# Performance work log

Hardware: AMD Instinct MI355X
Metric: run time of the kernel (lower is better)

The kernel has to match this reference:

```python
import jax, jax.numpy as jnp
import numpy as np

DIM = 512; LAYERS = 6; K = 15; VOCAB = 32000; B = 2; L = 1024
HID = 1024  # SwiGLU hidden: int(512*2) rounded up to multiple of 64
RANK = 64; BLOCK = 2048; MIX_W = 0.1
UP_DIL = [1, 2, 4, 8, 16, 32]
DN_DIL = UP_DIL[::-1]


def rmsnorm(x, w, eps=1e-6):
    return x * jax.lax.rsqrt(jnp.mean(x * x, axis=-1, keepdims=True) + eps) * w


def dconv(x, w, b, dil):
    # x: [B,D,T]; w: [D,1,K] depthwise; left (causal) padding of (K-1)*dil
    pad = (w.shape[-1] - 1) * dil
    y = jax.lax.conv_general_dilated(
        x, w, window_strides=(1,), padding=[(pad, 0)], rhs_dilation=(dil,),
        dimension_numbers=('NCH', 'OIH', 'NCH'), feature_group_count=x.shape[1])
    return y + b[None, :, None]


def conv_block(x, nw, cw, cb, w1, w2, w3, dil):
    # CausalDilatedConv: RMSNorm -> depthwise causal dilated conv -> silu -> SwiGLU -> +residual
    h = rmsnorm(x, nw)
    h = jax.nn.silu(dconv(jnp.transpose(h, (0, 2, 1)), cw, cb, dil))
    h = jnp.transpose(h, (0, 2, 1))
    h = jnp.einsum('bth,dh->btd',
                   jax.nn.silu(jnp.einsum('btd,hd->bth', h, w1)) * jnp.einsum('btd,hd->bth', h, w3),
                   w2)
    return h + x


def run_stack(x, dils, nw, cw, cb, w1, w2, w3, kp, ki, kd, gnorm):
    integral = x; previous = x; current = x
    for i, d in enumerate(dils):
        if i > 0:
            # PIDGate: step == i >= 1 so max(step,1) == i
            pid = kp[i-1] * current + ki[i-1] * (integral / i) + kd[i-1] * (current - previous)
            cur_in = rmsnorm(jax.nn.silu(pid), gnorm[i-1])
        else:
            cur_in = current
        current = conv_block(cur_in, nw[i], cw[i], cb[i], w1[i], w2[i], w3[i], d)
        previous = current
        integral = integral + current
    return current


def mix(x):
    # CausalMeanPool: x + 0.1 * causal running mean
    counts = jnp.arange(1, x.shape[1] + 1, dtype=x.dtype)[None, :, None]
    return x + MIX_W * jnp.cumsum(x, axis=1) / counts


def sgate(new, old, nw, dw, db, uw, ub):
    h = jax.nn.silu(rmsnorm(new, nw) @ dw.T + db)
    g = jax.nn.sigmoid(h @ uw.T + ub)
    return g * new + (1.0 - g) * old


def setup_inputs() -> dict:
    key = jax.random.key(0)
    ks = iter(jax.random.split(key, 64))
    def nrm(shape, s=0.02):
        return jax.random.normal(next(ks), shape, jnp.float32) * s
    def stack_params(p):
        return {
            p + '_norm_w': jnp.ones((LAYERS, DIM), jnp.float32),
            p + '_conv_w': nrm((LAYERS, DIM, 1, K), 0.1),
            p + '_conv_b': jnp.zeros((LAYERS, DIM), jnp.float32),
            p + '_w1': nrm((LAYERS, HID, DIM)),
            p + '_w2': nrm((LAYERS, DIM, HID)),
            p + '_w3': nrm((LAYERS, HID, DIM)),
            p + '_kp': jnp.full((LAYERS - 1, DIM), 0.5, jnp.float32),
            p + '_ki': jnp.full((LAYERS - 1, DIM), 0.3, jnp.float32),
            p + '_kd': jnp.full((LAYERS - 1, DIM), 0.2, jnp.float32),
            p + '_gnorm': jnp.ones((LAYERS - 1, DIM), jnp.float32),
        }
    inp = {
        'idx': jax.random.randint(next(ks), (B, L), 0, VOCAB),
        'emb': nrm((VOCAB, DIM)),
        'pos': nrm((1, BLOCK, DIM)),
        'emb_norm_w': jnp.ones((DIM,), jnp.float32),
        'token_shift': jnp.full((DIM,), 0.5, jnp.float32),
        'mem_gate_w': jnp.zeros((DIM, DIM), jnp.float32),  # nn.init.zeros_
        'mem_gate_b': nrm((DIM,)),
        'memory_p': jnp.zeros((B, DIM), jnp.float32),  # buffer, zero after reset()
        'sg_norm': jnp.ones((3, DIM), jnp.float32),
        'sg_down_w': nrm((3, RANK, DIM)),
        'sg_down_b': jnp.zeros((3, RANK), jnp.float32),
        'sg_up_w': nrm((3, DIM, RANK)),
        'sg_up_b': jnp.zeros((3, DIM), jnp.float32),
        'final_norm_w': jnp.ones((DIM,), jnp.float32),
    }
    inp.update(stack_params('up'))
    inp.update(stack_params('dn'))
    return inp


def _forward(idx, emb, pos, emb_norm_w, token_shift, mem_gate_w, mem_gate_b, memory_p,
             up_norm_w, up_conv_w, up_conv_b, up_w1, up_w2, up_w3, up_kp, up_ki, up_kd, up_gnorm,
             dn_norm_w, dn_conv_w, dn_conv_b, dn_w1, dn_w2, dn_w3, dn_kp, dn_ki, dn_kd, dn_gnorm,
             sg_norm, sg_down_w, sg_down_b, sg_up_w, sg_up_b, final_norm_w):
    T = idx.shape[1]
    x = emb[idx] + pos[:, :T]
    x = rmsnorm(x, emb_norm_w)
    # dropout is identity at eval time
    # memory injection: token-shift mix + sigmoid-gated persistent P-memory
    shifted = jnp.concatenate(
        [x[:, :1], token_shift * x[:, :-1] + (1.0 - token_shift) * x[:, 1:]], axis=1)
    mem = jax.nn.sigmoid(memory_p @ mem_gate_w.T + mem_gate_b)
    x = shifted + mem[:, None, :]
    initial = x
    up_p = (up_norm_w, up_conv_w, up_conv_b, up_w1, up_w2, up_w3, up_kp, up_ki, up_kd, up_gnorm)
    dn_p = (dn_norm_w, dn_conv_w, dn_conv_b, dn_w1, dn_w2, dn_w3, dn_kp, dn_ki, dn_kd, dn_gnorm)
    up1 = mix(run_stack(x, UP_DIL, *up_p))
    gated1 = sgate(up1, initial, sg_norm[0], sg_down_w[0], sg_down_b[0], sg_up_w[0], sg_up_b[0])
    down = mix(run_stack(gated1, DN_DIL, *dn_p))
    gated2 = sgate(down, initial, sg_norm[1], sg_down_w[1], sg_down_b[1], sg_up_w[1], sg_up_b[1])
    up2 = mix(run_stack(gated2, UP_DIL, *up_p))  # up_stack weights are shared/reused
    output = sgate(up2, gated2, sg_norm[2], sg_down_w[2], sg_down_b[2], sg_up_w[2], sg_up_b[2])
    output = rmsnorm(output, final_norm_w)
    return output @ emb.T  # tied head


def reference(idx, emb, pos, emb_norm_w, token_shift, mem_gate_w, mem_gate_b, memory_p,
              up_norm_w, up_conv_w, up_conv_b, up_w1, up_w2, up_w3, up_kp, up_ki, up_kd, up_gnorm,
              dn_norm_w, dn_conv_w, dn_conv_b, dn_w1, dn_w2, dn_w3, dn_kp, dn_ki, dn_kd, dn_gnorm,
              sg_norm, sg_down_w, sg_down_b, sg_up_w, sg_up_b, final_norm_w):
    return _forward(idx, emb, pos, emb_norm_w, token_shift, mem_gate_w, mem_gate_b, memory_p,
                    up_norm_w, up_conv_w, up_conv_b, up_w1, up_w2, up_w3, up_kp, up_ki, up_kd, up_gnorm,
                    dn_norm_w, dn_conv_w, dn_conv_b, dn_w1, dn_w2, dn_w3, dn_kp, dn_ki, dn_kd, dn_gnorm,
                    sg_norm, sg_down_w, sg_down_b, sg_up_w, sg_up_b, final_norm_w)
```

## Files before the change

### kernel.cpp

```cpp
#include <hip/hip_runtime.h>
#include <math.h>

#define DIM 512
#define NLAYERS 6
#define KSZ 15
#define VOCAB 32000
#define BATCH 2
#define SEQ 1024
#define HIDN 1024
#define RANK 64
#define NTOK (BATCH*SEQ)
#define MIXW 0.1f

typedef unsigned short u16;
typedef _Float16 f16;
typedef _Float16 f16x8 __attribute__((ext_vector_type(8)));
typedef _Float16 f16x4 __attribute__((ext_vector_type(4)));
typedef float  f32x4  __attribute__((ext_vector_type(4)));

__device__ __forceinline__ float sigm(float x){ return 1.f/(1.f+__expf(-x)); }

__device__ __forceinline__ float wred(float v){
  #pragma unroll
  for (int o=32;o>0;o>>=1) v += __shfl_xor(v, o, 64);
  return v;
}

#define MFMA16(a,b,c) __builtin_amdgcn_mfma_f32_16x16x32_f16(a,b,c,0,0,0)

__device__ __forceinline__ void gld16(const f16* g, f16* l){
  __builtin_amdgcn_global_load_lds(
      (const __attribute__((address_space(1))) void*)g,
      (__attribute__((address_space(3))) void*)l, 16, 0, 0);
}

__global__ __launch_bounds__(256) void k_cvt(const float* __restrict__ s,
    f16* __restrict__ d, long n4){
  long i = (long)blockIdx.x*256 + threadIdx.x;
  if (i >= n4) return;
  float4 v = reinterpret_cast<const float4*>(s)[i];
  f16x4 o; o.x=(f16)v.x; o.y=(f16)v.y; o.z=(f16)v.z; o.w=(f16)v.w;
  reinterpret_cast<f16x4*>(d)[i] = o;
}

__global__ __launch_bounds__(256) void k_cvtconv(const float* __restrict__ cw,
    float* __restrict__ cwT, int n){
  int i = blockIdx.x*256 + threadIdx.x;
  if (i >= n) return;
  int d = i & (DIM-1); int m = (i >> 9) % KSZ; int l = i / (KSZ*DIM);
  cwT[i] = cw[((size_t)l*DIM + d)*KSZ + (KSZ-1-m)];
}

__global__ __launch_bounds__(64) void k_embnorm(const int* __restrict__ idx,
    const float* __restrict__ emb, const float* __restrict__ pos,
    const float* __restrict__ w, float* __restrict__ out){
  int row = blockIdx.x;
  int t = row & (SEQ-1);
  int lane = threadIdx.x;
  long ebase = (long)idx[row]*DIM;
  long pbase = (long)t*DIM;
  float v[8]; float ss = 0.f;
  #pragma unroll
  for (int c=0;c<2;c++){
    int d = c*256 + lane*4;
    float4 e = *reinterpret_cast<const float4*>(emb + ebase + d);
    float4 p = *reinterpret_cast<const float4*>(pos + pbase + d);
    float x0 = e.x+p.x, x1 = e.y+p.y, x2 = e.z+p.z, x3 = e.w+p.w;
    v[c*4+0]=x0; v[c*4+1]=x1; v[c*4+2]=x2; v[c*4+3]=x3;
    ss += x0*x0 + x1*x1 + x2*x2 + x3*x3;
  }
  ss = wred(ss);
  float rs = rsqrtf(ss*(1.f/DIM) + 1e-6f);
  long ob = (long)row*DIM;
  #pragma unroll
  for (int c=0;c<2;c++){
    int d = c*256 + lane*4;
    float4 wv = *reinterpret_cast<const float4*>(w + d);
    float4 o;
    o.x = v[c*4+0]*rs*wv.x; o.y = v[c*4+1]*rs*wv.y;
    o.z = v[c*4+2]*rs*wv.z; o.w = v[c*4+3]*rs*wv.w;
    *reinterpret_cast<float4*>(out + ob + d) = o;
  }
}

__global__ void k_mem(const float* __restrict__ p, const float* __restrict__ gw,
                      const float* __restrict__ gb, float* __restrict__ mem){
  int i = blockIdx.x*blockDim.x + threadIdx.x;
  if (i >= BATCH*DIM) return;
  int b = i >> 9, d = i & (DIM-1);
  float acc = gb[d];
  const float* wr = gw + (long)d*DIM;
  const float* pr = p + b*DIM;
  for (int k=0;k<DIM;k+=4){
    float4 wv = *reinterpret_cast<const float4*>(wr+k);
    float4 pv = *reinterpret_cast<const float4*>(pr+k);
    acc += wv.x*pv.x + wv.y*pv.y + wv.z*pv.z + wv.w*pv.w;
  }
  mem[i] = sigm(acc);
}

__global__ void k_shift(const float* __restrict__ xn, const float* __restrict__ mem,
    const float* __restrict__ ts, float* __restrict__ out){
  int i = blockIdx.x*256 + threadIdx.x;
  int d = i & (DIM-1); int row = i >> 9; int t = row & (SEQ-1); int b = row >> 10;
  float cur = xn[i];
  float v;
  if (t == 0) v = cur;
  else { float f = ts[d]; v = f*xn[i-DIM] + (1.f-f)*cur; }
  out[i] = v + mem[b*DIM + d];
}

__global__ __launch_bounds__(64) void k_rms(const float* __restrict__ x,
    const float* __restrict__ w, f16* __restrict__ oh){
  int row = blockIdx.x; int lane = threadIdx.x;
  const float* xr = x + (long)row*DIM;
  float v[8]; float ss = 0.f;
  #pragma unroll
  for (int c=0;c<2;c++){
    int d = c*256 + lane*4;
    float4 f = *reinterpret_cast<const float4*>(xr + d);
    v[c*4+0]=f.x; v[c*4+1]=f.y; v[c*4+2]=f.z; v[c*4+3]=f.w;
    ss += f.x*f.x + f.y*f.y + f.z*f.z + f.w*f.w;
  }
  ss = wred(ss);
  float rs = rsqrtf(ss*(1.f/DIM) + 1e-6f);
  long ob = (long)row*DIM;
  #pragma unroll
  for (int c=0;c<2;c++){
    int d = c*256 + lane*4;
    float4 wv = *reinterpret_cast<const float4*>(w + d);
    f16x4 o;
    o.x = (f16)(v[c*4+0]*rs*wv.x); o.y = (f16)(v[c*4+1]*rs*wv.y);
    o.z = (f16)(v[c*4+2]*rs*wv.z); o.w = (f16)(v[c*4+3]*rs*wv.w);
    *reinterpret_cast<f16x4*>(oh + ob + d) = o;
  }
}

__global__ __launch_bounds__(64) void k_pid(const float* __restrict__ C,
    const float* __restrict__ I, float inv_i,
    const float* __restrict__ kp, const float* __restrict__ ki,
    const float* __restrict__ gn, const float* __restrict__ nw,
    float* __restrict__ xin, f16* __restrict__ oh){
  int row = blockIdx.x; int lane = threadIdx.x;
  long base = (long)row*DIM;
  float u[8]; float ss = 0.f;
  #pragma unroll
  for (int c=0;c<2;c++){
    int d = c*256 + lane*4;
    float4 cv = *reinterpret_cast<const float4*>(C + base + d);
    float4 iv = *reinterpret_cast<const float4*>(I + base + d);
    float4 kpv = *reinterpret_cast<const float4*>(kp + d);
    float4 kiv = *reinterpret_cast<const float4*>(ki + d);
    float p0 = kpv.x*cv.x + kiv.x*(iv.x*inv_i);
    float p1 = kpv.y*cv.y + kiv.y*(iv.y*inv_i);
    float p2 = kpv.z*cv.z + kiv.z*(iv.z*inv_i);
    float p3 = kpv.w*cv.w + kiv.w*(iv.w*inv_i);
    float s0 = p0*sigm(p0), s1 = p1*sigm(p1), s2 = p2*sigm(p2), s3 = p3*sigm(p3);
    u[c*4+0]=s0; u[c*4+1]=s1; u[c*4+2]=s2; u[c*4+3]=s3;
    ss += s0*s0 + s1*s1 + s2*s2 + s3*s3;
  }
  ss = wred(ss);
  float rs1 = rsqrtf(ss*(1.f/DIM) + 1e-6f);
  float x2[8]; float ss2 = 0.f;
  #pragma unroll
  for (int c=0;c<2;c++){
    int d = c*256 + lane*4;
    float4 gv = *reinterpret_cast<const float4*>(gn + d);
    float y0 = u[c*4+0]*rs1*gv.x, y1 = u[c*4+1]*rs1*gv.y;
    float y2 = u[c*4+2]*rs1*gv.z, y3 = u[c*4+3]*rs1*gv.w;
    x2[c*4+0]=y0; x2[c*4+1]=y1; x2[c*4+2]=y2; x2[c*4+3]=y3;
    ss2 += y0*y0 + y1*y1 + y2*y2 + y3*y3;
    float4 o; o.x=y0; o.y=y1; o.z=y2; o.w=y3;
    *reinterpret_cast<float4*>(xin + base + d) = o;
  }
  ss2 = wred(ss2);
  float rs2 = rsqrtf(ss2*(1.f/DIM) + 1e-6f);
  #pragma unroll
  for (int c=0;c<2;c++){
    int d = c*256 + lane*4;
    float4 nv = *reinterpret_cast<const float4*>(nw + d);
    f16x4 o;
    o.x = (f16)(x2[c*4+0]*rs2*nv.x); o.y = (f16)(x2[c*4+1]*rs2*nv.y);
    o.z = (f16)(x2[c*4+2]*rs2*nv.z); o.w = (f16)(x2[c*4+3]*rs2*nv.w);
    *reinterpret_cast<f16x4*>(oh + base + d) = o;
  }
}

__global__ void k_conv(const f16* __restrict__ h1,
    const float* __restrict__ cwT, const float* __restrict__ cb,
    f16* __restrict__ hc, int dil){
  int i = blockIdx.x*256 + threadIdx.x;
  int d = i & (DIM-1); int row = i >> 9; int t = row & (SEQ-1);
  float acc = cb[d];
  #pragma unroll
  for (int m=0;m<KSZ;m++){
    if (t - m*dil >= 0) acc += cwT[m*DIM + d] * (float)h1[i - m*dil*DIM];
  }
  float s = acc * sigm(acc);
  hc[i] = (f16)s;
}

template<int BM,int KD,int EPI>
__global__ __launch_bounds__(256) void k_mm(
    const f16* __restrict__ A, const f16* __restrict__ B0, const f16* __restrict__ B1,
    const float* __restrict__ XIN, float* __restrict__ OF, float* __restrict__ I,
    f16* __restrict__ OH){
  constexpr int WM = BM/4, MF = WM/16, NF = 4;
  constexpr int NMAT = (EPI==0) ? 2 : 1;
  constexpr int ATILE = BM*64;
  constexpr int BTILE = NMAT*64*64;
  constexpr int STRIDE = ATILE + BTILE;
  constexpr int AI = (BM/4)/8;
  constexpr int NT = KD/64;
  __shared__ f16 smem[2*STRIDE];
  int tid = threadIdx.x;
  int lane = tid & 63, wid = tid >> 6;
  int m0, n0;
  if constexpr (EPI==2){ int bid = blockIdx.x; m0 = (bid&15)*BM; n0 = (bid>>4)*64; }
  else { m0 = blockIdx.x*BM; n0 = blockIdx.y*64; }

  int lrow = lane >> 3, slot = lane & 7;

  auto stage = [&](int buf, int k0){
    f16* sA = smem + buf*STRIDE;
    f16* sB = sA + ATILE;
    #pragma unroll
    for (int j=0;j<AI;j++){
      int rowb = wid*(BM/4) + j*8;
      int row = rowb + lrow;
      gld16(A + (size_t)(m0+row)*KD + k0 + ((slot^(row&7))*8), sA + rowb*64);
    }
    #pragma unroll
    for (int j=0;j<2;j++){
      int rowb = wid*16 + j*8;
      int row = rowb + lrow;
      gld16(B0 + (size_t)(n0+row)*KD + k0 + ((slot^(row&7))*8), sB + rowb*64);
      if constexpr (EPI==0)
        gld16(B1 + (size_t)(n0+row)*KD + k0 + ((slot^(row&7))*8), sB + 4096 + rowb*64);
    }
  };

  f32x4 acc0[MF][NF] = {};
  f32x4 acc1[(EPI==0)?MF:1][(EPI==0)?NF:1] = {};

  stage(0, 0);
  __syncthreads();
  for (int t=0;t<NT;t++){
    int cur = t & 1;
    if (t+1 < NT) stage(cur^1, (t+1)*64);
    const f16* sA = smem + cur*STRIDE;
    const f16* sB = sA + ATILE;
    #pragma unroll
    for (int kk=0;kk<2;kk++){
      int kp0 = kk*4 + (lane>>4);
      f16x8 af[MF], bf[NF], bg[(EPI==0)?NF:1];
      #pragma unroll
      for (int mf=0;mf<MF;mf++){
        int row = wid*WM + mf*16 + (lane&15);
        af[mf] = *reinterpret_cast<const f16x8*>(&sA[row*64 + (kp0^(row&7))*8]);
      }
      #pragma unroll
      for (int nf=0;nf<NF;nf++){
        int row = nf*16 + (lane&15);
        bf[nf] = *reinterpret_cast<const f16x8*>(&sB[row*64 + (kp0^(row&7))*8]);
        if constexpr (EPI==0)
          bg[nf] = *reinterpret_cast<const f16x8*>(&sB[4096 + row*64 + (kp0^(row&7))*8]);
      }
      #pragma unroll
      for (int mf=0;mf<MF;mf++){
        #pragma unroll
        for (int nf=0;nf<NF;nf++){
          acc0[mf][nf] = MFMA16(af[mf], bf[nf], acc0[mf][nf]);
          if constexpr (EPI==0)
            acc1[mf][nf] = MFMA16(af[mf], bg[nf], acc1[mf][nf]);
        }
      }
    }
    __syncthreads();
  }

  float* stg = (float*)smem + wid*(16*68);
  int dr = (lane>>4)*4, dc = lane&15;
  #pragma unroll
  for (int mf=0;mf<MF;mf++){
    #pragma unroll
    for (int nf=0;nf<NF;nf++){
      #pragma unroll
      for (int q=0;q<4;q++){
        float v;
        if constexpr (EPI==0){
          float x1 = acc0[mf][nf][q];
          v = x1*sigm(x1)*acc1[mf][nf][q];
        } else v = acc0[mf][nf][q];
        stg[(dr+q)*68 + nf*16 + dc] = v;
      }
    }
    int gmb = m0 + wid*WM + mf*16;
    if constexpr (EPI==0){
      #pragma unroll
      for (int pass=0;pass<2;pass++){
        int r = pass*8 + (lane>>3);
        int c = 8*(lane&7);
        float4 lo = *reinterpret_cast<float4*>(&stg[r*68 + c]);
        float4 hi = *reinterpret_cast<float4*>(&stg[r*68 + c + 4]);
        f16x8 o;
        o[0]=(f16)lo.x; o[1]=(f16)lo.y; o[2]=(f16)lo.z; o[3]=(f16)lo.w;
        o[4]=(f16)hi.x; o[5]=(f16)hi.y; o[6]=(f16)hi.z; o[7]=(f16)hi.w;
        *reinterpret_cast<f16x8*>(&OH[(size_t)(gmb+r)*HIDN + n0 + c]) = o;
      }
    } else if constexpr (EPI==1){
      #pragma unroll
      for (int pass=0;pass<4;pass++){
        int r = pass*4 + (lane>>4);
        int c = 4*(lane&15);
        float4 v = *reinterpret_cast<float4*>(&stg[r*68 + c]);
        size_t o = (size_t)(gmb+r)*DIM + n0 + c;
        float4 x = *reinterpret_cast<const float4*>(&XIN[o]);
        v.x += x.x; v.y += x.y; v.z += x.z; v.w += x.w;
        *reinterpret_cast<float4*>(&OF[o]) = v;
        float4 iv = *reinterpret_cast<const float4*>(&I[o]);
        iv.x += v.x; iv.y += v.y; iv.z += v.z; iv.w += v.w;
        *reinterpret_cast<float4*>(&I[o]) = iv;
      }
    } else {
      #pragma unroll
      for (int pass=0;pass<4;pass++){
        int r = pass*4 + (lane>>4);
        int c = 4*(lane&15);
        float4 v = *reinterpret_cast<float4*>(&stg[r*68 + c]);
        *reinterpret_cast<float4*>(&OF[(size_t)(gmb+r)*VOCAB + n0 + c]) = v;
      }
    }
  }
}

__global__ __launch_bounds__(64) void k_mix(float* __restrict__ x){
  int col = blockIdx.x;
  int b = col >> 9, d = col & (DIM-1);
  int lane = threadIdx.x;
  long o = (long)b*SEQ*DIM + d + (long)lane*16*DIM;
  float v[16]; float s = 0.f;
  #pragma unroll
  for (int j=0;j<16;j++){ v[j] = x[o + (long)j*DIM]; s += v[j]; }
  float t = s;
  #pragma unroll
  for (int off=1; off<64; off<<=1){
    float u = __shfl_up(t, off, 64);
    if (lane >= off) t += u;
  }
  float run = t - s;
  #pragma unroll
  for (int j=0;j<16;j++){
    run += v[j];
    int tt = lane*16 + j;
    x[o + (long)j*DIM] = v[j] + MIXW*run/(float)(tt+1);
  }
}

__global__ __launch_bounds__(256) void k_sgate(const float* __restrict__ xnew,
    const float* __restrict__ xold, const float* __restrict__ nw,
    const float* __restrict__ dw, const float* __restrict__ db,
    const float* __restrict__ uw, const float* __restrict__ ub,
    float* __restrict__ out){
  __shared__ float raw[DIM];
  __shared__ float xn[DIM];
  __shared__ float part[256];
  __shared__ float hb[RANK];
  int row = blockIdx.x, tid = threadIdx.x;
  long base = (long)row*DIM;
  float ss = 0.f;
  for (int d=tid; d<DIM; d+=256){ float v = xnew[base+d]; raw[d]=v; ss += v*v; }
  ss = wred(ss);
  if ((tid&63)==0) part[tid>>6] = ss;
  __syncthreads();
  float tot = part[0]+part[1]+part[2]+part[3];
  float rs = rsqrtf(tot*(1.f/DIM)+1e-6f);
  for (int d=tid; d<DIM; d+=256) xn[d] = raw[d]*rs*nw[d];
  __syncthreads();
  int rr = tid & 63, q = tid >> 6;
  float p = 0.f;
  const float* dwr = dw + (long)rr*DIM + q*128;
  const float* xq = xn + q*128;
  #pragma unroll 8
  for (int d=0; d<128; d+=4){
    float4 wv = *reinterpret_cast<const float4*>(dwr+d);
    p += xq[d]*wv.x + xq[d+1]*wv.y + xq[d+2]*wv.z + xq[d+3]*wv.w;
  }
  part[tid] = p;
  __syncthreads();
  if (tid < RANK){
    float h = part[tid] + part[64+tid] + part[128+tid] + part[192+tid] + db[tid];
    hb[tid] = h * sigm(h);
  }
  __syncthreads();
  for (int d=tid; d<DIM; d+=256){
    float a = ub[d];
    const float* ur = uw + (long)d*RANK;
    #pragma unroll
    for (int rj=0;rj<RANK;rj+=4){
      float4 uv = *reinterpret_cast<const float4*>(ur+rj);
      a += hb[rj]*uv.x + hb[rj+1]*uv.y + hb[rj+2]*uv.z + hb[rj+3]*uv.w;
    }
    float g = sigm(a);
    out[base+d] = g*raw[d] + (1.f-g)*xold[base+d];
  }
}

extern "C" void kernel_launch(void* const* d_in, const int* in_sizes, int n_in,
                              void* d_out, int out_size, void* d_ws, size_t ws_size,
                              hipStream_t stream){
  const int*   idx           = (const int*)d_in[0];
  const float* emb           = (const float*)d_in[1];
  const float* pos           = (const float*)d_in[2];
  const float* emb_norm_w    = (const float*)d_in[3];
  const float* token_shift   = (const float*)d_in[4];
  const float* mem_gate_w    = (const float*)d_in[5];
  const float* mem_gate_b    = (const float*)d_in[6];
  const float* memory_p      = (const float*)d_in[7];
  const float* sg_norm       = (const float*)d_in[8];
  const float* sg_down_w     = (const float*)d_in[9];
  const float* sg_down_b     = (const float*)d_in[10];
  const float* sg_up_w       = (const float*)d_in[11];
  const float* sg_up_b       = (const float*)d_in[12];
  const float* final_norm_w  = (const float*)d_in[13];
  struct StackP { const float *nw, *cw, *cb, *w1, *w2, *w3, *kp, *ki, *gn; };
  StackP up { (const float*)d_in[14], (const float*)d_in[15], (const float*)d_in[16],
              (const float*)d_in[17], (const float*)d_in[18], (const float*)d_in[19],
              (const float*)d_in[20], (const float*)d_in[21], (const float*)d_in[23] };
  StackP dn { (const float*)d_in[24], (const float*)d_in[25], (const float*)d_in[26],
              (const float*)d_in[27], (const float*)d_in[28], (const float*)d_in[29],
              (const float*)d_in[30], (const float*)d_in[31], (const float*)d_in[33] };

  char* wp = (char*)d_ws;
  auto alloc = [&](size_t bytes)->void*{
    void* p = (void*)wp; wp += (bytes + 255) & ~(size_t)255; return p;
  };
  float* A0  = (float*)alloc((size_t)NTOK*DIM*4);
  float* A1  = (float*)alloc((size_t)NTOK*DIM*4);
  float* Cb  = (float*)alloc((size_t)NTOK*DIM*4);
  float* Ib  = (float*)alloc((size_t)NTOK*DIM*4);
  float* XIN = (float*)alloc((size_t)NTOK*DIM*4);
  f16*   H1  = (f16*)alloc((size_t)NTOK*DIM*2);
  f16*   HC  = (f16*)alloc((size_t)NTOK*DIM*2);
  f16*   G   = (f16*)alloc((size_t)NTOK*HIDN*2);
  const size_t WSZ = (size_t)NLAYERS*HIDN*DIM;
  f16*   UpW1 = (f16*)alloc(WSZ*2);
  f16*   UpW2 = (f16*)alloc(WSZ*2);
  f16*   UpW3 = (f16*)alloc(WSZ*2);
  f16*   DnW1 = (f16*)alloc(WSZ*2);
  f16*   DnW2 = (f16*)alloc(WSZ*2);
  f16*   DnW3 = (f16*)alloc(WSZ*2);
  f16*   Ef   = (f16*)alloc((size_t)VOCAB*DIM*2);
  float* UpCT = (float*)alloc((size_t)NLAYERS*KSZ*DIM*4);
  float* DnCT = (float*)alloc((size_t)NLAYERS*KSZ*DIM*4);
  float* MEM  = (float*)alloc((size_t)BATCH*DIM*4);

  static const int updil[NLAYERS] = {1,2,4,8,16,32};
  static const int dndil[NLAYERS] = {32,16,8,4,2,1};

  {
    long n4 = WSZ/4;
    int g = (int)((n4 + 255)/256);
    k_cvt<<<g,256,0,stream>>>(up.w1, UpW1, n4);
    k_cvt<<<g,256,0,stream>>>(up.w2, UpW2, n4);
    k_cvt<<<g,256,0,stream>>>(up.w3, UpW3, n4);
    k_cvt<<<g,256,0,stream>>>(dn.w1, DnW1, n4);
    k_cvt<<<g,256,0,stream>>>(dn.w2, DnW2, n4);
    k_cvt<<<g,256,0,stream>>>(dn.w3, DnW3, n4);
    long e4 = (long)VOCAB*DIM/4;
    k_cvt<<<(int)((e4+255)/256),256,0,stream>>>(emb, Ef, e4);
    int nc = NLAYERS*KSZ*DIM;
    k_cvtconv<<<(nc+255)/256,256,0,stream>>>(up.cw, UpCT, nc);
    k_cvtconv<<<(nc+255)/256,256,0,stream>>>(dn.cw, DnCT, nc);
  }

  k_embnorm<<<NTOK,64,0,stream>>>(idx, emb, pos, emb_norm_w, Cb);
  k_mem<<<(BATCH*DIM+255)/256,256,0,stream>>>(memory_p, mem_gate_w, mem_gate_b, MEM);
  k_shift<<<NTOK*DIM/256,256,0,stream>>>(Cb, MEM, token_shift, A0);

  auto run_stack = [&](const float* xs, const StackP& S, const float* CT,
                       const f16* W1f, const f16* W2f, const f16* W3f, const int* dil){
    hipMemcpyAsync(Ib, xs, (size_t)NTOK*DIM*4, hipMemcpyDeviceToDevice, stream);
    for (int l=0;l<NLAYERS;l++){
      const float* bin;
      if (l==0){
        bin = xs;
        k_rms<<<NTOK,64,0,stream>>>(xs, S.nw + l*DIM, H1);
      } else {
        k_pid<<<NTOK,64,0,stream>>>(Cb, Ib, 1.f/(float)l,
            S.kp+(l-1)*DIM, S.ki+(l-1)*DIM, S.gn+(l-1)*DIM, S.nw+l*DIM, XIN, H1);
        bin = XIN;
      }
      k_conv<<<NTOK*DIM/256,256,0,stream>>>(H1, CT + (size_t)l*KSZ*DIM, S.cb + l*DIM, HC, dil[l]);
      k_mm<128,512,0><<<dim3(NTOK/128, HIDN/64),256,0,stream>>>(
          HC, W1f + (size_t)l*HIDN*DIM, W3f + (size_t)l*HIDN*DIM,
          nullptr, nullptr, nullptr, G);
      k_mm<64,1024,1><<<dim3(NTOK/64, DIM/64),256,0,stream>>>(
          G, W2f + (size_t)l*DIM*HIDN, nullptr,
          bin, Cb, Ib, nullptr);
    }
  };

  run_stack(A0, up, UpCT, UpW1, UpW2, UpW3, updil);
  k_mix<<<BATCH*DIM,64,0,stream>>>(Cb);
  k_sgate<<<NTOK,256,0,stream>>>(Cb, A0, sg_norm, sg_down_w, sg_down_b, sg_up_w, sg_up_b, A1);
  run_stack(A1, dn, DnCT, DnW1, DnW2, DnW3, dndil);
  k_mix<<<BATCH*DIM,64,0,stream>>>(Cb);
  k_sgate<<<NTOK,256,0,stream>>>(Cb, A0, sg_norm+DIM, sg_down_w+RANK*DIM, sg_down_b+RANK,
                                 sg_up_w+DIM*RANK, sg_up_b+DIM, A1);
  run_stack(A1, up, UpCT, UpW1, UpW2, UpW3, updil);
  k_mix<<<BATCH*DIM,64,0,stream>>>(Cb);
  k_sgate<<<NTOK,256,0,stream>>>(Cb, A1, sg_norm+2*DIM, sg_down_w+2*RANK*DIM, sg_down_b+2*RANK,
                                 sg_up_w+2*DIM*RANK, sg_up_b+2*DIM, Cb);
  k_rms<<<NTOK,64,0,stream>>>(Cb, final_norm_w, H1);
  k_mm<128,512,2><<<16*(VOCAB/64),256,0,stream>>>(
      H1, Ef, nullptr, nullptr, (float*)d_out, nullptr, nullptr);
}
```

Baseline: 1.093 ms.

## Rewrite GEMMs with 8-wave blocks, direct A loads, and vectorize conv

```diff
diff --git a/kernel.cpp b/kernel.cpp
--- a/kernel.cpp
+++ b/kernel.cpp
@@ -186,150 +186,273 @@
   }
 }
 
-__global__ void k_conv(const f16* __restrict__ h1,
+__global__ __launch_bounds__(256) void k_conv(const f16* __restrict__ h1,
     const float* __restrict__ cwT, const float* __restrict__ cb,
     f16* __restrict__ hc, int dil){
   int i = blockIdx.x*256 + threadIdx.x;
-  int d = i & (DIM-1); int row = i >> 9; int t = row & (SEQ-1);
-  float acc = cb[d];
+  int d8 = (i & 63) << 3; int row = i >> 6; int t = row & (SEQ-1);
+  float acc[8];
+  {
+    float4 b0 = *reinterpret_cast<const float4*>(&cb[d8]);
+    float4 b1 = *reinterpret_cast<const float4*>(&cb[d8+4]);
+    acc[0]=b0.x; acc[1]=b0.y; acc[2]=b0.z; acc[3]=b0.w;
+    acc[4]=b1.x; acc[5]=b1.y; acc[6]=b1.z; acc[7]=b1.w;
+  }
   #pragma unroll
   for (int m=0;m<KSZ;m++){
-    if (t - m*dil >= 0) acc += cwT[m*DIM + d] * (float)h1[i - m*dil*DIM];
-  }
-  float s = acc * sigm(acc);
-  hc[i] = (f16)s;
-}
-
-template<int BM,int KD,int EPI>
-__global__ __launch_bounds__(256) void k_mm(
-    const f16* __restrict__ A, const f16* __restrict__ B0, const f16* __restrict__ B1,
-    const float* __restrict__ XIN, float* __restrict__ OF, float* __restrict__ I,
-    f16* __restrict__ OH){
-  constexpr int WM = BM/4, MF = WM/16, NF = 4;
-  constexpr int NMAT = (EPI==0) ? 2 : 1;
-  constexpr int ATILE = BM*64;
-  constexpr int BTILE = NMAT*64*64;
-  constexpr int STRIDE = ATILE + BTILE;
-  constexpr int AI = (BM/4)/8;
-  constexpr int NT = KD/64;
-  __shared__ f16 smem[2*STRIDE];
-  int tid = threadIdx.x;
-  int lane = tid & 63, wid = tid >> 6;
-  int m0, n0;
-  if constexpr (EPI==2){ int bid = blockIdx.x; m0 = (bid&15)*BM; n0 = (bid>>4)*64; }
-  else { m0 = blockIdx.x*BM; n0 = blockIdx.y*64; }
-
-  int lrow = lane >> 3, slot = lane & 7;
-
-  auto stage = [&](int buf, int k0){
-    f16* sA = smem + buf*STRIDE;
-    f16* sB = sA + ATILE;
-    #pragma unroll
-    for (int j=0;j<AI;j++){
-      int rowb = wid*(BM/4) + j*8;
-      int row = rowb + lrow;
-      gld16(A + (size_t)(m0+row)*KD + k0 + ((slot^(row&7))*8), sA + rowb*64);
-    }
+    if (t - m*dil >= 0){
+      f16x8 h = *reinterpret_cast<const f16x8*>(&h1[(size_t)(row - m*dil)*DIM + d8]);
+      float4 w0 = *reinterpret_cast<const float4*>(&cwT[m*DIM + d8]);
+      float4 w1 = *reinterpret_cast<const float4*>(&cwT[m*DIM + d8 + 4]);
+      acc[0]+=w0.x*(float)h[0]; acc[1]+=w0.y*(float)h[1];
+      acc[2]+=w0.z*(float)h[2]; acc[3]+=w0.w*(float)h[3];
+      acc[4]+=w1.x*(float)h[4]; acc[5]+=w1.y*(float)h[5];
+      acc[6]+=w1.z*(float)h[6]; acc[7]+=w1.w*(float)h[7];
+    }
+  }
+  f16x8 o;
+  #pragma unroll
+  for (int j=0;j<8;j++){ o[j] = (f16)(acc[j]*sigm(acc[j])); }
+  *reinterpret_cast<f16x8*>(&hc[(size_t)row*DIM + d8]) = o;
+}
+
+
+__global__ __launch_bounds__(512) void k_dual(const f16* __restrict__ A,
+    const f16* __restrict__ W1, const f16* __restrict__ W3, f16* __restrict__ G){
+  __shared__ __align__(16) char smemc[50176];
+  f16*   sB   = (f16*)smemc;
+  float* stgf = (float*)smemc;
+  float* kred = (float*)smemc + 4352;
+  int tid = threadIdx.x, lane = tid&63, wid = tid>>6;
+  int wk = wid>>2, wm = wid&3;
+  int m0 = blockIdx.x*128, n0 = blockIdx.y*64;
+  int r16 = lane&15, kq = lane>>4;
+
+  auto stage = [&](int buf, int t){
     #pragma unroll
     for (int j=0;j<2;j++){
-      int rowb = wid*16 + j*8;
-      int row = rowb + lrow;
-      gld16(B0 + (size_t)(n0+row)*KD + k0 + ((slot^(row&7))*8), sB + rowb*64);
-      if constexpr (EPI==0)
-        gld16(B1 + (size_t)(n0+row)*KD + k0 + ((slot^(row&7))*8), sB + 4096 + rowb*64);
+      int cc = j*512 + tid;
+      int mat = cc>>9, c2 = cc&511, r = c2>>3, s = c2&7;
+      const f16* src = (mat ? W3 : W1) + (size_t)(n0+r)*512 + t*64 + ((s^(r&7))<<3);
+      gld16(src, sB + buf*8192 + (j*512 + wid*64)*8);
     }
   };
 
-  f32x4 acc0[MF][NF] = {};
-  f32x4 acc1[(EPI==0)?MF:1][(EPI==0)?NF:1] = {};
-
+  f32x4 acc[2][4] = {};
   stage(0, 0);
   __syncthreads();
-  for (int t=0;t<NT;t++){
-    int cur = t & 1;
-    if (t+1 < NT) stage(cur^1, (t+1)*64);
-    const f16* sA = smem + cur*STRIDE;
-    const f16* sB = sA + ATILE;
+  #pragma unroll
+  for (int t=0;t<8;t++){
+    if (t < 7) stage((t&1)^1, t+1);
+    f16x8 af[2][2];
+    #pragma unroll
+    for (int kk=0;kk<2;kk++)
+      #pragma unroll
+      for (int mf=0;mf<2;mf++){
+        int row = m0 + wm*32 + mf*16 + r16;
+        af[kk][mf] = *reinterpret_cast<const f16x8*>(A + (size_t)row*512 + t*64 + (kk*4+kq)*8);
+      }
+    const f16* sbt = sB + (t&1)*8192 + wk*4096;
     #pragma unroll
     for (int kk=0;kk<2;kk++){
-      int kp0 = kk*4 + (lane>>4);
-      f16x8 af[MF], bf[NF], bg[(EPI==0)?NF:1];
-      #pragma unroll
-      for (int mf=0;mf<MF;mf++){
-        int row = wid*WM + mf*16 + (lane&15);
-        af[mf] = *reinterpret_cast<const f16x8*>(&sA[row*64 + (kp0^(row&7))*8]);
+      int kp0 = kk*4 + kq;
+      f16x8 bf[4];
+      #pragma unroll
+      for (int nf=0;nf<4;nf++){
+        int row = nf*16 + r16;
+        bf[nf] = *reinterpret_cast<const f16x8*>(&sbt[row*64 + ((kp0^(row&7))<<3)]);
       }
       #pragma unroll
-      for (int nf=0;nf<NF;nf++){
-        int row = nf*16 + (lane&15);
-        bf[nf] = *reinterpret_cast<const f16x8*>(&sB[row*64 + (kp0^(row&7))*8]);
-        if constexpr (EPI==0)
-          bg[nf] = *reinterpret_cast<const f16x8*>(&sB[4096 + row*64 + (kp0^(row&7))*8]);
+      for (int mf=0;mf<2;mf++)
+        #pragma unroll
+        for (int nf=0;nf<4;nf++)
+          acc[mf][nf] = MFMA16(af[kk][mf], bf[nf], acc[mf][nf]);
+    }
+    __syncthreads();
+  }
+  if (wk == 1){
+    #pragma unroll
+    for (int mf=0;mf<2;mf++)
+      #pragma unroll
+      for (int nf=0;nf<4;nf++)
+        *reinterpret_cast<f32x4*>(&kred[(((wm*2+mf)*4+nf)<<8) + lane*4]) = acc[mf][nf];
+  }
+  __syncthreads();
+  if (wk == 1) return;
+  int dr = (lane>>4)*4, dc = lane&15;
+  float* stg = stgf + wm*1088;
+  #pragma unroll
+  for (int mf=0;mf<2;mf++){
+    #pragma unroll
+    for (int nf=0;nf<4;nf++){
+      f32x4 a3 = *reinterpret_cast<f32x4*>(&kred[(((wm*2+mf)*4+nf)<<8) + lane*4]);
+      #pragma unroll
+      for (int q=0;q<4;q++){
+        float x1 = acc[mf][nf][q];
+        stg[(dr+q)*68 + nf*16 + dc] = x1*sigm(x1)*a3[q];
       }
-      #pragma unroll
-      for (int mf=0;mf<MF;mf++){
+    }
+    int gmb = m0 + wm*32 + mf*16;
+    #pragma unroll
+    for (int pass=0;pass<2;pass++){
+      int rr = pass*8 + (lane>>3), c = 8*(lane&7);
+      float4 lo = *reinterpret_cast<float4*>(&stg[rr*68 + c]);
+      float4 hi = *reinterpret_cast<float4*>(&stg[rr*68 + c + 4]);
+      f16x8 o;
+      o[0]=(f16)lo.x; o[1]=(f16)lo.y; o[2]=(f16)lo.z; o[3]=(f16)lo.w;
+      o[4]=(f16)hi.x; o[5]=(f16)hi.y; o[6]=(f16)hi.z; o[7]=(f16)hi.w;
+      *reinterpret_cast<f16x8*>(&G[(size_t)(gmb+rr)*HIDN + n0 + c]) = o;
+    }
+  }
+}
+
+__global__ __launch_bounds__(512) void k_w2(const f16* __restrict__ A,
+    const f16* __restrict__ W, const float* __restrict__ XIN,
+    float* __restrict__ OF, float* __restrict__ I, int init){
+  __shared__ __align__(16) char smemc[33792];
+  f16*   sB   = (f16*)smemc;
+  float* stgf = (float*)smemc;
+  float* kred = (float*)smemc + 4352;
+  int tid = threadIdx.x, lane = tid&63, wid = tid>>6;
+  int wk = wid>>2, wm = wid&3;
+  int m0 = blockIdx.x*64, n0 = blockIdx.y*64;
+  int r16 = lane&15, kq = lane>>4;
+
+  auto stage = [&](int buf, int t){
+    #pragma unroll
+    for (int j=0;j<2;j++){
+      int cc = j*512 + tid;
+      int kg = cc>>9, c2 = cc&511, r = c2>>3, s = c2&7;
+      const f16* src = W + (size_t)(n0+r)*1024 + kg*512 + t*64 + ((s^(r&7))<<3);
+      gld16(src, sB + buf*8192 + (j*512 + wid*64)*8);
+    }
+  };
+
+  f32x4 acc[4] = {};
+  stage(0, 0);
+  __syncthreads();
+  #pragma unroll
+  for (int t=0;t<8;t++){
+    if (t < 7) stage((t&1)^1, t+1);
+    f16x8 af[2];
+    #pragma unroll
+    for (int kk=0;kk<2;kk++){
+      int row = m0 + wm*16 + r16;
+      af[kk] = *reinterpret_cast<const f16x8*>(A + (size_t)row*1024 + wk*512 + t*64 + (kk*4+kq)*8);
+    }
+    const f16* sbt = sB + (t&1)*8192 + wk*4096;
+    #pragma unroll
+    for (int kk=0;kk<2;kk++){
+      int kp0 = kk*4 + kq;
+      #pragma unroll
+      for (int nf=0;nf<4;nf++){
+        int row = nf*16 + r16;
+        f16x8 bf = *reinterpret_cast<const f16x8*>(&sbt[row*64 + ((kp0^(row&7))<<3)]);
+        acc[nf] = MFMA16(af[kk], bf, acc[nf]);
+      }
+    }
+    __syncthreads();
+  }
+  if (wk == 1){
+    #pragma unroll
+    for (int nf=0;nf<4;nf++)
+      *reinterpret_cast<f32x4*>(&kred[((wm*4+nf)<<8) + lane*4]) = acc[nf];
+  }
+  __syncthreads();
+  if (wk == 1) return;
+  #pragma unroll
+  for (int nf=0;nf<4;nf++){
+    f32x4 p = *reinterpret_cast<f32x4*>(&kred[((wm*4+nf)<<8) + lane*4]);
+    acc[nf][0]+=p[0]; acc[nf][1]+=p[1]; acc[nf][2]+=p[2]; acc[nf][3]+=p[3];
+  }
+  int dr = (lane>>4)*4, dc = lane&15;
+  float* stg = stgf + wm*1088;
+  #pragma unroll
+  for (int nf=0;nf<4;nf++)
+    #pragma unroll
+    for (int q=0;q<4;q++)
+      stg[(dr+q)*68 + nf*16 + dc] = acc[nf][q];
+  int gmb = m0 + wm*16;
+  #pragma unroll
+  for (int pass=0;pass<4;pass++){
+    int rr = pass*4 + (lane>>4), c = 4*(lane&15);
+    float4 v = *reinterpret_cast<float4*>(&stg[rr*68 + c]);
+    size_t o = (size_t)(gmb+rr)*DIM + n0 + c;
+    float4 x = *reinterpret_cast<const float4*>(&XIN[o]);
+    v.x+=x.x; v.y+=x.y; v.z+=x.z; v.w+=x.w;
+    *reinterpret_cast<float4*>(&OF[o]) = v;
+    float4 iv;
+    if (init) iv = x;
+    else      iv = *reinterpret_cast<const float4*>(&I[o]);
+    iv.x+=v.x; iv.y+=v.y; iv.z+=v.z; iv.w+=v.w;
+    *reinterpret_cast<float4*>(&I[o]) = iv;
+  }
+}
+
+__global__ __launch_bounds__(512) void k_logits(const f16* __restrict__ A,
+    const f16* __restrict__ E, float* __restrict__ OF){
+  __shared__ __align__(16) char smemc[34816];
+  f16*   sB   = (f16*)smemc;
+  float* stgf = (float*)smemc;
+  int tid = threadIdx.x, lane = tid&63, wid = tid>>6;
+  int bid = blockIdx.x;
+  int m0 = (bid&7)*256, n0 = (bid>>3)*64;
+  int r16 = lane&15, kq = lane>>4;
+
+  auto stage = [&](int buf, int t){
+    int cc = tid;
+    int r = cc>>3, s = cc&7;
+    const f16* src = E + (size_t)(n0+r)*512 + t*64 + ((s^(r&7))<<3);
+    gld16(src, sB + buf*4096 + wid*64*8);
+  };
+
+  f32x4 acc[2][4] = {};
+  stage(0, 0);
+  __syncthreads();
+  #pragma unroll
+  for (int t=0;t<8;t++){
+    if (t < 7) stage((t&1)^1, t+1);
+    f16x8 af[2][2];
+    #pragma unroll
+    for (int kk=0;kk<2;kk++)
+      #pragma unroll
+      for (int mf=0;mf<2;mf++){
+        int row = m0 + wid*32 + mf*16 + r16;
+        af[kk][mf] = *reinterpret_cast<const f16x8*>(A + (size_t)row*512 + t*64 + (kk*4+kq)*8);
+      }
+    const f16* sbt = sB + (t&1)*4096;
+    #pragma unroll
+    for (int kk=0;kk<2;kk++){
+      int kp0 = kk*4 + kq;
+      f16x8 bf[4];
+      #pragma unroll
+      for (int nf=0;nf<4;nf++){
+        int row = nf*16 + r16;
+        bf[nf] = *reinterpret_cast<const f16x8*>(&sbt[row*64 + ((kp0^(row&7))<<3)]);
+      }
+      #pragma unroll
+      for (int mf=0;mf<2;mf++)
         #pragma unroll
-        for (int nf=0;nf<NF;nf++){
-          acc0[mf][nf] = MFMA16(af[mf], bf[nf], acc0[mf][nf]);
-          if constexpr (EPI==0)
-            acc1[mf][nf] = MFMA16(af[mf], bg[nf], acc1[mf][nf]);
-        }
-      }
+        for (int nf=0;nf<4;nf++)
+          acc[mf][nf] = MFMA16(af[kk][mf], bf[nf], acc[mf][nf]);
     }
     __syncthreads();
   }
-
-  float* stg = (float*)smem + wid*(16*68);
   int dr = (lane>>4)*4, dc = lane&15;
-  #pragma unroll
-  for (int mf=0;mf<MF;mf++){
-    #pragma unroll
-    for (int nf=0;nf<NF;nf++){
-      #pragma unroll
-      for (int q=0;q<4;q++){
-        float v;
-        if constexpr (EPI==0){
-          float x1 = acc0[mf][nf][q];
-          v = x1*sigm(x1)*acc1[mf][nf][q];
-        } else v = acc0[mf][nf][q];
-        stg[(dr+q)*68 + nf*16 + dc] = v;
-      }
-    }
-    int gmb = m0 + wid*WM + mf*16;
-    if constexpr (EPI==0){
-      #pragma unroll
-      for (int pass=0;pass<2;pass++){
-        int r = pass*8 + (lane>>3);
-        int c = 8*(lane&7);
-        float4 lo = *reinterpret_cast<float4*>(&stg[r*68 + c]);
-        float4 hi = *reinterpret_cast<float4*>(&stg[r*68 + c + 4]);
-        f16x8 o;
-        o[0]=(f16)lo.x; o[1]=(f16)lo.y; o[2]=(f16)lo.z; o[3]=(f16)lo.w;
-        o[4]=(f16)hi.x; o[5]=(f16)hi.y; o[6]=(f16)hi.z; o[7]=(f16)hi.w;
-        *reinterpret_cast<f16x8*>(&OH[(size_t)(gmb+r)*HIDN + n0 + c]) = o;
-      }
-    } else if constexpr (EPI==1){
-      #pragma unroll
-      for (int pass=0;pass<4;pass++){
-        int r = pass*4 + (lane>>4);
-        int c = 4*(lane&15);
-        float4 v = *reinterpret_cast<float4*>(&stg[r*68 + c]);
-        size_t o = (size_t)(gmb+r)*DIM + n0 + c;
-        float4 x = *reinterpret_cast<const float4*>(&XIN[o]);
-        v.x += x.x; v.y += x.y; v.z += x.z; v.w += x.w;
-        *reinterpret_cast<float4*>(&OF[o]) = v;
-        float4 iv = *reinterpret_cast<const float4*>(&I[o]);
-        iv.x += v.x; iv.y += v.y; iv.z += v.z; iv.w += v.w;
-        *reinterpret_cast<float4*>(&I[o]) = iv;
-      }
-    } else {
-      #pragma unroll
-      for (int pass=0;pass<4;pass++){
-        int r = pass*4 + (lane>>4);
-        int c = 4*(lane&15);
-        float4 v = *reinterpret_cast<float4*>(&stg[r*68 + c]);
-        *reinterpret_cast<float4*>(&OF[(size_t)(gmb+r)*VOCAB + n0 + c]) = v;
-      }
+  float* stg = stgf + wid*1088;
+  #pragma unroll
+  for (int mf=0;mf<2;mf++){
+    #pragma unroll
+    for (int nf=0;nf<4;nf++)
+      #pragma unroll
+      for (int q=0;q<4;q++)
+        stg[(dr+q)*68 + nf*16 + dc] = acc[mf][nf][q];
+    int gmb = m0 + wid*32 + mf*16;
+    #pragma unroll
+    for (int pass=0;pass<4;pass++){
+      int rr = pass*4 + (lane>>4), c = 4*(lane&15);
+      float4 v = *reinterpret_cast<float4*>(&stg[rr*68 + c]);
+      *reinterpret_cast<float4*>(&OF[(size_t)(gmb+rr)*VOCAB + n0 + c]) = v;
     }
   }
 }
@@ -480,7 +603,6 @@
 
   auto run_stack = [&](const float* xs, const StackP& S, const float* CT,
                        const f16* W1f, const f16* W2f, const f16* W3f, const int* dil){
-    hipMemcpyAsync(Ib, xs, (size_t)NTOK*DIM*4, hipMemcpyDeviceToDevice, stream);
     for (int l=0;l<NLAYERS;l++){
       const float* bin;
       if (l==0){
@@ -491,13 +613,11 @@
             S.kp+(l-1)*DIM, S.ki+(l-1)*DIM, S.gn+(l-1)*DIM, S.nw+l*DIM, XIN, H1);
         bin = XIN;
       }
-      k_conv<<<NTOK*DIM/256,256,0,stream>>>(H1, CT + (size_t)l*KSZ*DIM, S.cb + l*DIM, HC, dil[l]);
-      k_mm<128,512,0><<<dim3(NTOK/128, HIDN/64),256,0,stream>>>(
-          HC, W1f + (size_t)l*HIDN*DIM, W3f + (size_t)l*HIDN*DIM,
-          nullptr, nullptr, nullptr, G);
-      k_mm<64,1024,1><<<dim3(NTOK/64, DIM/64),256,0,stream>>>(
-          G, W2f + (size_t)l*DIM*HIDN, nullptr,
-          bin, Cb, Ib, nullptr);
+      k_conv<<<NTOK*DIM/8/256,256,0,stream>>>(H1, CT + (size_t)l*KSZ*DIM, S.cb + l*DIM, HC, dil[l]);
+      k_dual<<<dim3(NTOK/128, HIDN/64),512,0,stream>>>(
+          HC, W1f + (size_t)l*HIDN*DIM, W3f + (size_t)l*HIDN*DIM, G);
+      k_w2<<<dim3(NTOK/64, DIM/64),512,0,stream>>>(
+          G, W2f + (size_t)l*DIM*HIDN, bin, Cb, Ib, (l==0)?1:0);
     }
   };
 
@@ -513,6 +633,5 @@
   k_sgate<<<NTOK,256,0,stream>>>(Cb, A1, sg_norm+2*DIM, sg_down_w+2*RANK*DIM, sg_down_b+2*RANK,
                                  sg_up_w+2*DIM*RANK, sg_up_b+2*DIM, Cb);
   k_rms<<<NTOK,64,0,stream>>>(Cb, final_norm_w, H1);
-  k_mm<128,512,2><<<16*(VOCAB/64),256,0,stream>>>(
-      H1, Ef, nullptr, nullptr, (float*)d_out, nullptr, nullptr);
-}
+  k_logits<<<8*(VOCAB/64),512,0,stream>>>(H1, Ef, (float*)d_out);
+}
```

New measurement: 1.222 ms. 11.9% more time.

## Vectorize depthwise conv, batch weight conversions, fold integral init into GEMM

Applied to the files above, without the earlier changes.

```diff
diff --git a/kernel.cpp b/kernel.cpp
--- a/kernel.cpp
+++ b/kernel.cpp
@@ -34,6 +34,27 @@
       (__attribute__((address_space(3))) void*)l, 16, 0, 0);
 }
 
+__global__ __launch_bounds__(256) void k_cvt6(
+    const float* __restrict__ s0, const float* __restrict__ s1, const float* __restrict__ s2,
+    const float* __restrict__ s3, const float* __restrict__ s4, const float* __restrict__ s5,
+    f16* __restrict__ d0, f16* __restrict__ d1, f16* __restrict__ d2,
+    f16* __restrict__ d3, f16* __restrict__ d4, f16* __restrict__ d5, long n4){
+  long i = (long)blockIdx.x*256 + threadIdx.x;
+  if (i >= n4) return;
+  const float* s; f16* d;
+  switch (blockIdx.y){
+    case 0: s=s0; d=d0; break;
+    case 1: s=s1; d=d1; break;
+    case 2: s=s2; d=d2; break;
+    case 3: s=s3; d=d3; break;
+    case 4: s=s4; d=d4; break;
+    default: s=s5; d=d5; break;
+  }
+  float4 v = reinterpret_cast<const float4*>(s)[i];
+  f16x4 o; o.x=(f16)v.x; o.y=(f16)v.y; o.z=(f16)v.z; o.w=(f16)v.w;
+  reinterpret_cast<f16x4*>(d)[i] = o;
+}
+
 __global__ __launch_bounds__(256) void k_cvt(const float* __restrict__ s,
     f16* __restrict__ d, long n4){
   long i = (long)blockIdx.x*256 + threadIdx.x;
@@ -43,10 +64,12 @@
   reinterpret_cast<f16x4*>(d)[i] = o;
 }
 
-__global__ __launch_bounds__(256) void k_cvtconv(const float* __restrict__ cw,
-    float* __restrict__ cwT, int n){
+__global__ __launch_bounds__(256) void k_cvtconv2(const float* __restrict__ cwu,
+    const float* __restrict__ cwd, float* __restrict__ cwTu, float* __restrict__ cwTd, int n){
   int i = blockIdx.x*256 + threadIdx.x;
   if (i >= n) return;
+  const float* cw = blockIdx.y ? cwd : cwu;
+  float* cwT      = blockIdx.y ? cwTd : cwTu;
   int d = i & (DIM-1); int m = (i >> 9) % KSZ; int l = i / (KSZ*DIM);
   cwT[i] = cw[((size_t)l*DIM + d)*KSZ + (KSZ-1-m)];
 }
@@ -186,25 +209,41 @@
   }
 }
 
-__global__ void k_conv(const f16* __restrict__ h1,
+__global__ __launch_bounds__(256) void k_conv(const f16* __restrict__ h1,
     const float* __restrict__ cwT, const float* __restrict__ cb,
     f16* __restrict__ hc, int dil){
   int i = blockIdx.x*256 + threadIdx.x;
-  int d = i & (DIM-1); int row = i >> 9; int t = row & (SEQ-1);
-  float acc = cb[d];
+  int d8 = (i & 63) << 3; int row = i >> 6; int t = row & (SEQ-1);
+  float acc[8];
+  {
+    float4 b0 = *reinterpret_cast<const float4*>(&cb[d8]);
+    float4 b1 = *reinterpret_cast<const float4*>(&cb[d8+4]);
+    acc[0]=b0.x; acc[1]=b0.y; acc[2]=b0.z; acc[3]=b0.w;
+    acc[4]=b1.x; acc[5]=b1.y; acc[6]=b1.z; acc[7]=b1.w;
+  }
   #pragma unroll
   for (int m=0;m<KSZ;m++){
-    if (t - m*dil >= 0) acc += cwT[m*DIM + d] * (float)h1[i - m*dil*DIM];
-  }
-  float s = acc * sigm(acc);
-  hc[i] = (f16)s;
+    if (t - m*dil >= 0){
+      f16x8 h = *reinterpret_cast<const f16x8*>(&h1[(size_t)(row - m*dil)*DIM + d8]);
+      float4 w0 = *reinterpret_cast<const float4*>(&cwT[m*DIM + d8]);
+      float4 w1 = *reinterpret_cast<const float4*>(&cwT[m*DIM + d8 + 4]);
+      acc[0]+=w0.x*(float)h[0]; acc[1]+=w0.y*(float)h[1];
+      acc[2]+=w0.z*(float)h[2]; acc[3]+=w0.w*(float)h[3];
+      acc[4]+=w1.x*(float)h[4]; acc[5]+=w1.y*(float)h[5];
+      acc[6]+=w1.z*(float)h[6]; acc[7]+=w1.w*(float)h[7];
+    }
+  }
+  f16x8 o;
+  #pragma unroll
+  for (int j=0;j<8;j++){ o[j] = (f16)(acc[j]*sigm(acc[j])); }
+  *reinterpret_cast<f16x8*>(&hc[(size_t)row*DIM + d8]) = o;
 }
 
 template<int BM,int KD,int EPI>
 __global__ __launch_bounds__(256) void k_mm(
     const f16* __restrict__ A, const f16* __restrict__ B0, const f16* __restrict__ B1,
     const float* __restrict__ XIN, float* __restrict__ OF, float* __restrict__ I,
-    f16* __restrict__ OH){
+    f16* __restrict__ OH, int init){
   constexpr int WM = BM/4, MF = WM/16, NF = 4;
   constexpr int NMAT = (EPI==0) ? 2 : 1;
   constexpr int ATILE = BM*64;
@@ -318,7 +357,9 @@
         float4 x = *reinterpret_cast<const float4*>(&XIN[o]);
         v.x += x.x; v.y += x.y; v.z += x.z; v.w += x.w;
         *reinterpret_cast<float4*>(&OF[o]) = v;
-        float4 iv = *reinterpret_cast<const float4*>(&I[o]);
+        float4 iv;
+        if (init) iv = x;
+        else      iv = *reinterpret_cast<const float4*>(&I[o]);
         iv.x += v.x; iv.y += v.y; iv.z += v.z; iv.w += v.w;
         *reinterpret_cast<float4*>(&I[o]) = iv;
       }
@@ -461,17 +502,12 @@
   {
     long n4 = WSZ/4;
     int g = (int)((n4 + 255)/256);
-    k_cvt<<<g,256,0,stream>>>(up.w1, UpW1, n4);
-    k_cvt<<<g,256,0,stream>>>(up.w2, UpW2, n4);
-    k_cvt<<<g,256,0,stream>>>(up.w3, UpW3, n4);
-    k_cvt<<<g,256,0,stream>>>(dn.w1, DnW1, n4);
-    k_cvt<<<g,256,0,stream>>>(dn.w2, DnW2, n4);
-    k_cvt<<<g,256,0,stream>>>(dn.w3, DnW3, n4);
+    k_cvt6<<<dim3(g,6),256,0,stream>>>(up.w1, up.w2, up.w3, dn.w1, dn.w2, dn.w3,
+                                       UpW1, UpW2, UpW3, DnW1, DnW2, DnW3, n4);
     long e4 = (long)VOCAB*DIM/4;
     k_cvt<<<(int)((e4+255)/256),256,0,stream>>>(emb, Ef, e4);
     int nc = NLAYERS*KSZ*DIM;
-    k_cvtconv<<<(nc+255)/256,256,0,stream>>>(up.cw, UpCT, nc);
-    k_cvtconv<<<(nc+255)/256,256,0,stream>>>(dn.cw, DnCT, nc);
+    k_cvtconv2<<<dim3((nc+255)/256,2),256,0,stream>>>(up.cw, dn.cw, UpCT, DnCT, nc);
   }
 
   k_embnorm<<<NTOK,64,0,stream>>>(idx, emb, pos, emb_norm_w, Cb);
@@ -480,7 +516,6 @@
 
   auto run_stack = [&](const float* xs, const StackP& S, const float* CT,
                        const f16* W1f, const f16* W2f, const f16* W3f, const int* dil){
-    hipMemcpyAsync(Ib, xs, (size_t)NTOK*DIM*4, hipMemcpyDeviceToDevice, stream);
     for (int l=0;l<NLAYERS;l++){
       const float* bin;
       if (l==0){
@@ -491,13 +526,13 @@
             S.kp+(l-1)*DIM, S.ki+(l-1)*DIM, S.gn+(l-1)*DIM, S.nw+l*DIM, XIN, H1);
         bin = XIN;
       }
-      k_conv<<<NTOK*DIM/256,256,0,stream>>>(H1, CT + (size_t)l*KSZ*DIM, S.cb + l*DIM, HC, dil[l]);
+      k_conv<<<NTOK*DIM/8/256,256,0,stream>>>(H1, CT + (size_t)l*KSZ*DIM, S.cb + l*DIM, HC, dil[l]);
       k_mm<128,512,0><<<dim3(NTOK/128, HIDN/64),256,0,stream>>>(
           HC, W1f + (size_t)l*HIDN*DIM, W3f + (size_t)l*HIDN*DIM,
-          nullptr, nullptr, nullptr, G);
+          nullptr, nullptr, nullptr, G, 0);
       k_mm<64,1024,1><<<dim3(NTOK/64, DIM/64),256,0,stream>>>(
           G, W2f + (size_t)l*DIM*HIDN, nullptr,
-          bin, Cb, Ib, nullptr);
+          bin, Cb, Ib, nullptr, (l==0)?1:0);
     }
   };
 
@@ -514,5 +549,5 @@
                                  sg_up_w+2*DIM*RANK, sg_up_b+2*DIM, Cb);
   k_rms<<<NTOK,64,0,stream>>>(Cb, final_norm_w, H1);
   k_mm<128,512,2><<<16*(VOCAB/64),256,0,stream>>>(
-      H1, Ef, nullptr, nullptr, (float*)d_out, nullptr, nullptr);
-}
+      H1, Ef, nullptr, nullptr, (float*)d_out, nullptr, nullptr, 0);
+}
```

Result: faster. 1.060 ms (-3.0%).
